# Optimization experiments

Measured on AMD Instinct MI355X. Metric: run time of the kernel, lower is better.

Reference implementation:

```python
import jax, jax.numpy as jnp
import numpy as np

B, D, K, C = 512, 256, 65536, 1000
T_SUP, T_DC, LS = 0.07, 0.1, 0.1
EPS = 1e-8


def _l2norm(x, axis):
    return x / jnp.linalg.norm(x, axis=axis, keepdims=True)


def setup_inputs() -> dict:
    key = jax.random.key(0)
    k1, k2, k3, k4, k5, k6, k7, k8 = jax.random.split(key, 8)
    norm_q = _l2norm(jax.random.normal(k1, (B, D), jnp.float32), axis=1)
    k_feat = _l2norm(jax.random.normal(k2, (B, D), jnp.float32), axis=1)
    q_logits = jax.random.normal(k3, (B, C), jnp.float32)
    logits_k = jax.random.normal(k4, (B, C), jnp.float32)
    queue = _l2norm(jax.random.normal(k5, (D, K), jnp.float32), axis=0)
    # queue_label_prob stores softmaxed class-probabilities column-wise (prob.T)
    queue_label_prob = jax.nn.softmax(jax.random.normal(k6, (C, K), jnp.float32), axis=0)
    queue_label = jax.random.randint(k7, (K,), 0, C, jnp.int64)
    target = jax.random.randint(k8, (B,), 0, C, jnp.int64)
    return {
        "norm_q": norm_q, "q_logits": q_logits, "k_feat": k_feat,
        "logits_k": logits_k, "queue": queue,
        "queue_label_prob": queue_label_prob, "queue_label": queue_label,
        "target": target, "knn_k": 200,
    }


def reference(norm_q, q_logits, k_feat, logits_k, queue, queue_label_prob,
              queue_label, target, knn_k):
    b = norm_q.shape[0]

    # ---- supcon_in ----
    sim = norm_q @ queue                                  # [B, K]
    _, idx = jax.lax.top_k(sim, knn_k)                    # [B, knn_k]
    sim_knn = jnp.take_along_axis(sim, idx, axis=1)
    w = jax.nn.softmax(sim_knn / T_SUP, axis=-1)
    pos = (target[:, None] == queue_label[idx])           # [B, knn_k]
    gt = jnp.sum(w * pos, axis=1)                         # [B]
    m = gt > EPS
    supin_loss = jnp.sum(jnp.where(m, -jnp.log(jnp.where(m, gt, 1.0)), 0.0)) / b

    # ---- label-smoothed onehot ----
    onehot = jnp.full((b, C), LS / (C - 1), jnp.float32)
    onehot = onehot.at[jnp.arange(b), target].set(1.0 - LS)

    log_q = jax.nn.log_softmax(q_logits, axis=1)
    q_mask = jax.nn.softmax(q_logits, axis=1).min(axis=1) > EPS  # [B]

    # ---- fc loss (masked CE with label smoothing) ----
    fc_loss = -jnp.sum(jnp.sum(onehot * log_q, axis=1) * q_mask) / b

    # ---- generate_dc_target (no-grad in original) ----
    sim_k = jax.nn.softmax((k_feat @ queue) / T_DC, axis=-1)      # [B, K]
    dc_target = sim_k @ queue_label_prob.T                        # [B, C]

    # ---- dc loss: KL(dc_target || softmax(q_logits)), masked, sum / B ----
    kl = jnp.where(dc_target > 0, dc_target * (jnp.log(jnp.where(dc_target > 0, dc_target, 1.0)) - log_q), 0.0)
    dc_loss = jnp.sum(jnp.sum(kl, axis=1) * q_mask) / b

    return (supin_loss, fc_loss, dc_loss)
```

## Files before the change

kernel.cpp:

```cpp
#include <hip/hip_runtime.h>
#include <math.h>

#define BN 512
#define DN 256
#define KN 65536
#define CN 1000
#define EQ_CAP 512
#define EPSTR 136

typedef __attribute__((ext_vector_type(8))) short bf16x8;
typedef __attribute__((ext_vector_type(4))) float f32x4;

__device__ __forceinline__ unsigned short f2bf(float f) {
    unsigned u = __float_as_uint(f);
    unsigned r = (u + 0x7FFFu + ((u >> 16) & 1u)) >> 16;
    return (unsigned short)r;
}
__device__ __forceinline__ float bf2f(unsigned short h) {
    return __uint_as_float(((unsigned)h) << 16);
}
__device__ __forceinline__ unsigned fkey16(unsigned b) {
    b &= 0xFFFFu;
    return (b & 0x8000u) ? ((~b) & 0xFFFFu) : (b | 0x8000u);
}
__device__ __forceinline__ void async16(const void* g, void* l) {
    __builtin_amdgcn_global_load_lds(
        (const __attribute__((address_space(1))) unsigned*)g,
        (__attribute__((address_space(3))) unsigned*)l, 16, 0, 0);
}
__device__ __forceinline__ unsigned cvtpk(float lo, float hi) {
    unsigned r;
    asm("v_cvt_pk_bf16_f32 %0, %1, %2" : "=v"(r) : "v"(lo), "v"(hi));
    return r;
}

__global__ void __launch_bounds__(256) cvt_bf16(const float* __restrict__ in,
                                                unsigned short* __restrict__ out) {
    int i = (blockIdx.x * 256 + threadIdx.x) * 4;
    float4 v = *(const float4*)&in[i];
    ushort4 o;
    o.x = f2bf(v.x); o.y = f2bf(v.y); o.z = f2bf(v.z); o.w = f2bf(v.w);
    *(ushort4*)&out[i] = o;
}

__global__ void __launch_bounds__(256) transpose_q(const float* __restrict__ Q,
                                                   unsigned short* __restrict__ Qt) {
    __shared__ float T[64][65];
    int tid = threadIdx.x;
    int n0 = blockIdx.x * 64;
    int d0 = blockIdx.y * 64;
    #pragma unroll
    for (int i = 0; i < 4; ++i) {
        int flat = i * 256 + tid;
        int d = flat >> 4, nq = (flat & 15) * 4;
        float4 v = *(const float4*)&Q[(size_t)(d0 + d) * KN + n0 + nq];
        T[d][nq] = v.x; T[d][nq + 1] = v.y; T[d][nq + 2] = v.z; T[d][nq + 3] = v.w;
    }
    __syncthreads();
    int n = tid >> 2, dbase = (tid & 3) * 16;
    unsigned u[8];
    #pragma unroll
    for (int j = 0; j < 8; ++j) {
        unsigned short a = f2bf(T[dbase + 2 * j][n]);
        unsigned short b = f2bf(T[dbase + 2 * j + 1][n]);
        u[j] = (unsigned)a | ((unsigned)b << 16);
    }
    unsigned short* o = &Qt[(size_t)(n0 + n) * DN + d0 + dbase];
    *(uint4*)o = make_uint4(u[0], u[1], u[2], u[3]);
    *(uint4*)(o + 8) = make_uint4(u[4], u[5], u[6], u[7]);
}

__global__ void __launch_bounds__(256) gemm_sim(const unsigned short* __restrict__ A,
                                                const unsigned short* __restrict__ Bt,
                                                unsigned short* __restrict__ simOut,
                                                unsigned short* __restrict__ expOut,
                                                float* __restrict__ Zb,
                                                int mBlockSplit) {
    __shared__ unsigned short smem[128 * 64 * 2];
    __shared__ float Zred[128];
    unsigned short* As = smem;
    unsigned short* Bs = smem + 128 * 64;
    int tid = threadIdx.x;
    int n0 = blockIdx.x * 128, m0 = blockIdx.y * 128;
    bool isExp = ((int)blockIdx.y >= mBlockSplit);
    int lane = tid & 63, w = tid >> 6;
    int l15 = lane & 15, quad = lane >> 4;
    int wm = w & 1, wn = w >> 1;
    f32x4 acc[4][4];
    #pragma unroll
    for (int mi = 0; mi < 4; ++mi)
        #pragma unroll
        for (int ni = 0; ni < 4; ++ni)
            #pragma unroll
            for (int j = 0; j < 4; ++j) acc[mi][ni][j] = 0.f;

    for (int k0 = 0; k0 < DN; k0 += 64) {
        #pragma unroll
        for (int i = 0; i < 4; ++i) {
            int f = (i * 256 + tid) * 8;
            async16(A + (size_t)(m0 + (f >> 6)) * DN + k0 + (f & 63), &As[f]);
        }
        #pragma unroll
        for (int i = 0; i < 4; ++i) {
            int f = (i * 256 + tid) * 8;
            async16(Bt + (size_t)(n0 + (f >> 6)) * DN + k0 + (f & 63), &Bs[f]);
        }
        __syncthreads();
        #pragma unroll
        for (int ks = 0; ks < 2; ++ks) {
            bf16x8 am[4], bn[4];
            #pragma unroll
            for (int mi = 0; mi < 4; ++mi)
                am[mi] = *(const bf16x8*)&As[(wm * 64 + mi * 16 + l15) * 64 + ks * 32 + quad * 8];
            #pragma unroll
            for (int ni = 0; ni < 4; ++ni)
                bn[ni] = *(const bf16x8*)&Bs[(wn * 64 + ni * 16 + l15) * 64 + ks * 32 + quad * 8];
            #pragma unroll
            for (int mi = 0; mi < 4; ++mi)
                #pragma unroll
                for (int ni = 0; ni < 4; ++ni)
                    acc[mi][ni] = __builtin_amdgcn_mfma_f32_16x16x32_bf16(bn[ni], am[mi], acc[mi][ni], 0, 0, 0);
        }
        __syncthreads();
    }

    unsigned short* obase = isExp ? expOut : simOut;
    int orow0 = isExp ? (m0 - mBlockSplit * 128) : m0;
    float rsum[4] = {0.f, 0.f, 0.f, 0.f};

    #pragma unroll
    for (int round = 0; round < 2; ++round) {
        if (wm == round) {
            #pragma unroll
            for (int mi = 0; mi < 4; ++mi) {
                int mrow = mi * 16 + l15;
                #pragma unroll
                for (int ni = 0; ni < 4; ++ni) {
                    int nc = wn * 64 + ni * 16 + quad * 4;
                    float v0 = acc[mi][ni][0], v1 = acc[mi][ni][1];
                    float v2 = acc[mi][ni][2], v3 = acc[mi][ni][3];
                    if (isExp) {
                        v0 = __expf(v0 * 10.0f); v1 = __expf(v1 * 10.0f);
                        v2 = __expf(v2 * 10.0f); v3 = __expf(v3 * 10.0f);
                    }
                    unsigned short u0 = f2bf(v0), u1 = f2bf(v1), u2 = f2bf(v2), u3 = f2bf(v3);
                    if (isExp) rsum[mi] += bf2f(u0) + bf2f(u1) + bf2f(u2) + bf2f(u3);
                    *(uint2*)&smem[mrow * EPSTR + nc] =
                        make_uint2((unsigned)u0 | ((unsigned)u1 << 16),
                                   (unsigned)u2 | ((unsigned)u3 << 16));
                }
            }
        }
        __syncthreads();
        #pragma unroll
        for (int j = 0; j < 4; ++j) {
            int fc = j * 256 + tid;
            int mr = fc >> 4;
            int ch = fc & 15;
            uint4 val = *(uint4*)&smem[mr * EPSTR + ch * 8];
            int g = orow0 + round * 64 + mr;
            *(uint4*)&obase[(size_t)g * KN + n0 + ch * 8] = val;
        }
        __syncthreads();
    }

    if (isExp) {
        float v4[4];
        #pragma unroll
        for (int mi = 0; mi < 4; ++mi) {
            float v = rsum[mi];
            v += __shfl_xor(v, 16, 64);
            v += __shfl_xor(v, 32, 64);
            v4[mi] = v;
        }
        if (wn == 0 && quad == 0) {
            #pragma unroll
            for (int mi = 0; mi < 4; ++mi) Zred[wm * 64 + mi * 16 + l15] = v4[mi];
        }
        __syncthreads();
        if (wn == 1 && quad == 0) {
            #pragma unroll
            for (int mi = 0; mi < 4; ++mi) Zred[wm * 64 + mi * 16 + l15] += v4[mi];
        }
        __syncthreads();
        if (tid < 128) atomicAdd(&Zb[orow0 + tid], Zred[tid]);
    }
}

__global__ void __launch_bounds__(256) supcon(const unsigned short* __restrict__ sim,
                                              const int* __restrict__ qlabel,
                                              const int* __restrict__ target,
                                              const int* __restrict__ knnp,
                                              float* __restrict__ out0) {
    __shared__ unsigned hist[4][256];
    __shared__ unsigned s_sel, s_cntAbove;
    __shared__ int eqIdx[EQ_CAP];
    __shared__ unsigned eqCount;
    __shared__ float redZ[256], redN[256];
    int tid = threadIdx.x, w = tid >> 6;
    int row = blockIdx.x;
    const unsigned short* srow = sim + (size_t)row * KN;
    int knn = *knnp;
    int tgt = target[row];
    if (tid == 0) { eqCount = 0u; }
    #pragma unroll
    for (int j = 0; j < 4; ++j) hist[j][tid] = 0u;
    __syncthreads();
    for (int i0 = tid * 4; i0 < KN; i0 += 1024) {
        uint2 v = *(const uint2*)&srow[i0];
        atomicAdd(&hist[w][fkey16(v.x) >> 8], 1u);
        atomicAdd(&hist[w][fkey16(v.x >> 16) >> 8], 1u);
        atomicAdd(&hist[w][fkey16(v.y) >> 8], 1u);
        atomicAdd(&hist[w][fkey16(v.y >> 16) >> 8], 1u);
    }
    __syncthreads();
    if (tid == 0) {
        unsigned acc = 0; int chosen = 0;
        for (int bin = 255; bin >= 0; --bin) {
            unsigned h = hist[0][bin] + hist[1][bin] + hist[2][bin] + hist[3][bin];
            if (acc + h >= (unsigned)knn) { chosen = bin; break; }
            acc += h;
        }
        s_cntAbove = acc; s_sel = (unsigned)chosen;
    }
    __syncthreads();
    unsigned selHi = s_sel;
    #pragma unroll
    for (int j = 0; j < 4; ++j) hist[j][tid] = 0u;
    __syncthreads();
    for (int i0 = tid * 4; i0 < KN; i0 += 1024) {
        uint2 v = *(const uint2*)&srow[i0];
        unsigned k0 = fkey16(v.x), k1 = fkey16(v.x >> 16), k2 = fkey16(v.y), k3 = fkey16(v.y >> 16);
        if ((k0 >> 8) == selHi) atomicAdd(&hist[w][k0 & 255u], 1u);
        if ((k1 >> 8) == selHi) atomicAdd(&hist[w][k1 & 255u], 1u);
        if ((k2 >> 8) == selHi) atomicAdd(&hist[w][k2 & 255u], 1u);
        if ((k3 >> 8) == selHi) atomicAdd(&hist[w][k3 & 255u], 1u);
    }
    __syncthreads();
    if (tid == 0) {
        unsigned acc = s_cntAbove; int chosen = 0;
        for (int bin = 255; bin >= 0; --bin) {
            unsigned h = hist[0][bin] + hist[1][bin] + hist[2][bin] + hist[3][bin];
            if (acc + h >= (unsigned)knn) { chosen = bin; break; }
            acc += h;
        }
        s_cntAbove = acc; s_sel = (selHi << 8) | (unsigned)chosen;
    }
    __syncthreads();
    unsigned tu = s_sel;
    unsigned cgt = s_cntAbove;
    const float invT = 1.0f / 0.07f;
    float Zl = 0.f, Nl = 0.f;
    for (int i0 = tid * 4; i0 < KN; i0 += 1024) {
        uint2 v = *(const uint2*)&srow[i0];
        unsigned bits[4] = {v.x & 0xFFFFu, v.x >> 16, v.y & 0xFFFFu, v.y >> 16};
        #pragma unroll
        for (int j = 0; j < 4; ++j) {
            unsigned u = fkey16(bits[j]);
            if (u > tu) {
                float e = __expf(bf2f((unsigned short)bits[j]) * invT);
                Zl += e;
                if (qlabel[i0 + j] == tgt) Nl += e;
            } else if (u == tu) {
                unsigned pos = atomicAdd(&eqCount, 1u);
                if (pos < EQ_CAP) eqIdx[pos] = i0 + j;
            }
        }
    }
    redZ[tid] = Zl; redN[tid] = Nl;
    __syncthreads();
    for (int s = 128; s > 0; s >>= 1) {
        if (tid < s) { redZ[tid] += redZ[tid + s]; redN[tid] += redN[tid + s]; }
        __syncthreads();
    }
    if (tid == 0) {
        float Z = redZ[0], num = redN[0];
        int neq = (int)(eqCount < (unsigned)EQ_CAP ? eqCount : (unsigned)EQ_CAP);
        int needed = knn - (int)cgt;
        if (needed > neq) needed = neq;
        for (int a = 1; a < neq; ++a) {
            int v = eqIdx[a]; int b2 = a - 1;
            while (b2 >= 0 && eqIdx[b2] > v) { eqIdx[b2 + 1] = eqIdx[b2]; --b2; }
            eqIdx[b2 + 1] = v;
        }
        unsigned tb = (tu & 0x8000u) ? (tu & 0x7FFFu) : ((~tu) & 0xFFFFu);
        float wt = __expf(bf2f((unsigned short)tb) * invT);
        for (int a = 0; a < needed; ++a) {
            Z += wt;
            if (qlabel[eqIdx[a]] == tgt) num += wt;
        }
        float gt = num / Z;
        if (gt > 1e-8f) atomicAdd(out0, -logf(gt) * (1.0f / (float)BN));
    }
}

__global__ void __launch_bounds__(256, 3) dc_gemm(const unsigned short* __restrict__ E,
                                                  const float* __restrict__ P,
                                                  float* __restrict__ dct) {
    __shared__ unsigned short As[128 * 64];
    __shared__ float Bsf[128 * 64];
    int tid = threadIdx.x;
    int c0 = blockIdx.x * 128, m0 = blockIdx.y * 128;
    int kb = blockIdx.z * (KN / 32);
    int lane = tid & 63, w = tid >> 6;
    int l15 = lane & 15, quad = lane >> 4;
    int wm = w & 1, wn = w >> 1;
    int tr = tid >> 3, chA = tid & 7;
    int sa = (chA ^ (tr & 7)) << 3;
    int br = tid >> 4, cbB = tid & 15;
    int sb = (cbB ^ (br & 7)) << 2;
    const int swr = l15 & 7;
    f32x4 acc[4][4];
    #pragma unroll
    for (int r = 0; r < 4; ++r)
        #pragma unroll
        for (int c = 0; c < 4; ++c)
            #pragma unroll
            for (int j = 0; j < 4; ++j) acc[r][c][j] = 0.f;

    for (int kc = 0; kc < KN / 32; kc += 64) {
        #pragma unroll
        for (int i = 0; i < 4; ++i) {
            int row = i * 32 + tr;
            async16(E + (size_t)(m0 + row) * KN + kb + kc + sa, &As[(i * 256 + tid) * 8]);
        }
        #pragma unroll
        for (int i = 0; i < 8; ++i) {
            int gr = c0 + i * 16 + br;
            if (gr > CN - 1) gr = CN - 1;
            async16(P + (size_t)gr * KN + kb + kc + sb, &Bsf[(i * 256 + tid) * 4]);
        }
        __syncthreads();
        #pragma unroll
        for (int ks = 0; ks < 2; ++ks) {
            bf16x8 af[4], bfr[4];
            #pragma unroll
            for (int r = 0; r < 4; ++r) {
                int arow = wm * 64 + r * 16 + l15;
                af[r] = *(const bf16x8*)&As[arow * 64 + (((ks * 4 + quad) ^ swr) << 3)];
            }
            #pragma unroll
            for (int c = 0; c < 4; ++c) {
                int brow = wn * 64 + c * 16 + l15;
                int ck = ks * 8 + quad * 2;
                float4 ra = *(const float4*)&Bsf[brow * 64 + ((ck ^ swr) << 2)];
                float4 rb = *(const float4*)&Bsf[brow * 64 + (((ck + 1) ^ swr) << 2)];
                uint4 pk;
                pk.x = cvtpk(ra.x, ra.y); pk.y = cvtpk(ra.z, ra.w);
                pk.z = cvtpk(rb.x, rb.y); pk.w = cvtpk(rb.z, rb.w);
                bfr[c] = *(bf16x8*)&pk;
            }
            #pragma unroll
            for (int r = 0; r < 4; ++r)
                #pragma unroll
                for (int c = 0; c < 4; ++c)
                    acc[r][c] = __builtin_amdgcn_mfma_f32_16x16x32_bf16(af[r], bfr[c], acc[r][c], 0, 0, 0);
        }
        __syncthreads();
    }
    #pragma unroll
    for (int r = 0; r < 4; ++r)
        #pragma unroll
        for (int reg = 0; reg < 4; ++reg) {
            int m = m0 + wm * 64 + r * 16 + quad * 4 + reg;
            #pragma unroll
            for (int c = 0; c < 4; ++c) {
                int cc = c0 + wn * 64 + c * 16 + l15;
                atomicAdd(&dct[m * 1024 + cc], acc[r][c][reg]);
            }
        }
}

__global__ void __launch_bounds__(256) logq_fc(const float* __restrict__ x_all,
                                               const int* __restrict__ target,
                                               float* __restrict__ logq,
                                               float* __restrict__ qmask,
                                               float* __restrict__ out1) {
    int row = blockIdx.x, tid = threadIdx.x;
    const float* x = x_all + (size_t)row * CN;
    __shared__ float red[256], red2[256];
    float mx = -INFINITY, mn = INFINITY;
    for (int c = tid; c < CN; c += 256) { float v = x[c]; mx = fmaxf(mx, v); mn = fminf(mn, v); }
    red[tid] = mx; red2[tid] = mn;
    __syncthreads();
    for (int s = 128; s > 0; s >>= 1) {
        if (tid < s) { red[tid] = fmaxf(red[tid], red[tid + s]); red2[tid] = fminf(red2[tid], red2[tid + s]); }
        __syncthreads();
    }
    mx = red[0]; mn = red2[0];
    __syncthreads();
    float se = 0.f, sx = 0.f;
    for (int c = tid; c < CN; c += 256) { float v = x[c]; se += __expf(v - mx); sx += v; }
    red[tid] = se; red2[tid] = sx;
    __syncthreads();
    for (int s = 128; s > 0; s >>= 1) {
        if (tid < s) { red[tid] += red[tid + s]; red2[tid] += red2[tid + s]; }
        __syncthreads();
    }
    float lse = mx + logf(red[0]);
    float sumlogq = red2[0] - (float)CN * lse;
    for (int c = tid; c < CN; c += 256) logq[(size_t)row * CN + c] = x[c] - lse;
    if (tid == 0) {
        float lqt = x[target[row]] - lse;
        bool qm = (mn - lse) > logf(1e-8f);
        qmask[row] = qm ? 1.0f : 0.0f;
        if (qm) {
            float fc = -(0.1f / 999.0f * (sumlogq - lqt) + 0.9f * lqt);
            atomicAdd(out1, fc * (1.0f / (float)BN));
        }
    }
}

__global__ void __launch_bounds__(256) dc_loss(const float* __restrict__ dct,
                                               const float* __restrict__ logq,
                                               const float* __restrict__ qmask,
                                               const float* __restrict__ Z,
                                               float* __restrict__ out2) {
    int row = blockIdx.x, tid = threadIdx.x;
    __shared__ float red[256];
    float invZ = 1.0f / Z[row];
    float s = 0.f;
    for (int c = tid; c < CN; c += 256) {
        float T = dct[row * 1024 + c] * invZ;
        if (T > 0.f) s += T * (logf(T) - logq[(size_t)row * CN + c]);
    }
    red[tid] = s;
    __syncthreads();
    for (int st = 128; st > 0; st >>= 1) {
        if (tid < st) red[tid] += red[tid + st];
        __syncthreads();
    }
    if (tid == 0 && qmask[row] > 0.f)
        atomicAdd(out2, red[0] * (1.0f / (float)BN));
}

extern "C" void kernel_launch(void* const* d_in, const int* in_sizes, int n_in,
                              void* d_out, int out_size, void* d_ws, size_t ws_size,
                              hipStream_t stream) {
    (void)in_sizes; (void)n_in; (void)out_size;
    const float* norm_q   = (const float*)d_in[0];
    const float* q_logits = (const float*)d_in[1];
    const float* k_feat   = (const float*)d_in[2];
    const float* queue    = (const float*)d_in[4];
    const float* qlp      = (const float*)d_in[5];
    const int*   qlabel   = (const int*)d_in[6];
    const int*   target   = (const int*)d_in[7];
    const int*   knnp     = (const int*)d_in[8];
    float* out = (float*)d_out;
    char* ws = (char*)d_ws;

    const size_t SIM_B = 67108864;
    const size_t QT_B  = 33554432;
    const size_t AC_B  = 524288;
    const size_t FUSED_NEED = SIM_B * 2 + QT_B + AC_B + 2097152 + 2048 + 2048000 + 2048;
    bool fused = (ws_size >= FUSED_NEED);

    unsigned short *simBF, *Ebf, *queueT, *Acat;
    float *dct, *Zb, *logq, *qmask;
    if (fused) {
        simBF  = (unsigned short*)(ws);
        Ebf    = (unsigned short*)(ws + SIM_B);
        queueT = (unsigned short*)(ws + 2 * SIM_B);
        Acat   = (unsigned short*)(ws + 2 * SIM_B + QT_B);
        dct    = (float*)(ws + 2 * SIM_B + QT_B + AC_B);
    } else {
        simBF  = (unsigned short*)(ws);
        Ebf    = simBF;
        queueT = (unsigned short*)(ws + SIM_B);
        Acat   = (unsigned short*)(ws + SIM_B + QT_B);
        dct    = (float*)(ws + SIM_B + QT_B + AC_B);
    }
    Zb    = (float*)((char*)dct + 2097152);
    logq  = (float*)((char*)Zb + 2048);
    qmask = (float*)((char*)logq + 2048000);

    hipMemsetAsync(dct, 0, 2097152 + 2048, stream);
    hipMemsetAsync(d_out, 0, 3 * sizeof(float), stream);

    cvt_bf16<<<dim3(128), 256, 0, stream>>>(norm_q, Acat);
    cvt_bf16<<<dim3(128), 256, 0, stream>>>(k_feat, Acat + (size_t)BN * DN);
    transpose_q<<<dim3(KN / 64, 4), 256, 0, stream>>>(queue, queueT);

    if (fused) {
        gemm_sim<<<dim3(KN / 128, 8), 256, 0, stream>>>(Acat, queueT, simBF, Ebf, Zb, 4);
        supcon<<<dim3(BN), 256, 0, stream>>>(simBF, qlabel, target, knnp, out + 0);
    } else {
        gemm_sim<<<dim3(KN / 128, 4), 256, 0, stream>>>(Acat, queueT, simBF, nullptr, nullptr, 4);
        supcon<<<dim3(BN), 256, 0, stream>>>(simBF, qlabel, target, knnp, out + 0);
        gemm_sim<<<dim3(KN / 128, 4), 256, 0, stream>>>(Acat + (size_t)BN * DN, queueT,
                                                        nullptr, Ebf, Zb, 0);
    }
    dc_gemm<<<dim3(8, 4, 32), 256, 0, stream>>>(Ebf, qlp, dct);
    logq_fc<<<dim3(BN), 256, 0, stream>>>(q_logits, target, logq, qmask, out + 1);
    dc_loss<<<dim3(BN), 256, 0, stream>>>(dct, logq, qmask, Zb, out + 2);
}
```

Measured before the change: 748.2 us.

## Double-buffer dc_gemm shared-memory tiles with a K-step of 32

Measured after the change: 851.0 us. 13.7% more time.

```diff
diff --git a/kernel.cpp b/kernel.cpp
--- a/kernel.cpp
+++ b/kernel.cpp
@@ -297,19 +297,18 @@
 __global__ void __launch_bounds__(256, 3) dc_gemm(const unsigned short* __restrict__ E,
                                                   const float* __restrict__ P,
                                                   float* __restrict__ dct) {
-    __shared__ unsigned short As[128 * 64];
-    __shared__ float Bsf[128 * 64];
+    __shared__ unsigned short As[2][128 * 32];
+    __shared__ float Bsf[2][128 * 32];
     int tid = threadIdx.x;
     int c0 = blockIdx.x * 128, m0 = blockIdx.y * 128;
     int kb = blockIdx.z * (KN / 32);
     int lane = tid & 63, w = tid >> 6;
     int l15 = lane & 15, quad = lane >> 4;
     int wm = w & 1, wn = w >> 1;
-    int tr = tid >> 3, chA = tid & 7;
-    int sa = (chA ^ (tr & 7)) << 3;
-    int br = tid >> 4, cbB = tid & 15;
-    int sb = (cbB ^ (br & 7)) << 2;
-    const int swr = l15 & 7;
+    int tr = tid >> 2, chA = tid & 3;
+    int sa = (chA ^ ((tr >> 1) & 3)) << 3;
+    int br = tid >> 3, cb = tid & 7;
+    int sb = (cb ^ (br & 7)) << 2;
     f32x4 acc[4][4];
     #pragma unroll
     for (int r = 0; r < 4; ++r)
@@ -318,44 +317,48 @@
             #pragma unroll
             for (int j = 0; j < 4; ++j) acc[r][c][j] = 0.f;
 
-    for (int kc = 0; kc < KN / 32; kc += 64) {
+    auto stage = [&](int buf, int kpos) {
+        #pragma unroll
+        for (int i = 0; i < 2; ++i)
+            async16(E + (size_t)(m0 + i * 64 + tr) * KN + kpos + sa,
+                    &As[buf][(i * 256 + tid) * 8]);
         #pragma unroll
         for (int i = 0; i < 4; ++i) {
-            int row = i * 32 + tr;
-            async16(E + (size_t)(m0 + row) * KN + kb + kc + sa, &As[(i * 256 + tid) * 8]);
-        }
-        #pragma unroll
-        for (int i = 0; i < 8; ++i) {
-            int gr = c0 + i * 16 + br;
+            int gr = c0 + i * 32 + br;
             if (gr > CN - 1) gr = CN - 1;
-            async16(P + (size_t)gr * KN + kb + kc + sb, &Bsf[(i * 256 + tid) * 4]);
-        }
-        __syncthreads();
-        #pragma unroll
-        for (int ks = 0; ks < 2; ++ks) {
-            bf16x8 af[4], bfr[4];
-            #pragma unroll
-            for (int r = 0; r < 4; ++r) {
-                int arow = wm * 64 + r * 16 + l15;
-                af[r] = *(const bf16x8*)&As[arow * 64 + (((ks * 4 + quad) ^ swr) << 3)];
-            }
-            #pragma unroll
-            for (int c = 0; c < 4; ++c) {
-                int brow = wn * 64 + c * 16 + l15;
-                int ck = ks * 8 + quad * 2;
-                float4 ra = *(const float4*)&Bsf[brow * 64 + ((ck ^ swr) << 2)];
-                float4 rb = *(const float4*)&Bsf[brow * 64 + (((ck + 1) ^ swr) << 2)];
-                uint4 pk;
-                pk.x = cvtpk(ra.x, ra.y); pk.y = cvtpk(ra.z, ra.w);
-                pk.z = cvtpk(rb.x, rb.y); pk.w = cvtpk(rb.z, rb.w);
-                bfr[c] = *(bf16x8*)&pk;
-            }
-            #pragma unroll
-            for (int r = 0; r < 4; ++r)
-                #pragma unroll
-                for (int c = 0; c < 4; ++c)
-                    acc[r][c] = __builtin_amdgcn_mfma_f32_16x16x32_bf16(af[r], bfr[c], acc[r][c], 0, 0, 0);
-        }
+            async16(P + (size_t)gr * KN + kpos + sb, &Bsf[buf][(i * 256 + tid) * 4]);
+        }
+    };
+
+    stage(0, kb);
+    __syncthreads();
+    for (int t = 0; t < 64; ++t) {
+        int cur = t & 1;
+        if (t < 63) stage(cur ^ 1, kb + (t + 1) * 32);
+        const unsigned short* Ab = As[cur];
+        const float* Bb = Bsf[cur];
+        bf16x8 af[4], bfr[4];
+        #pragma unroll
+        for (int r = 0; r < 4; ++r) {
+            int arow = wm * 64 + r * 16 + l15;
+            af[r] = *(const bf16x8*)&Ab[arow * 32 + ((quad ^ ((arow >> 1) & 3)) << 3)];
+        }
+        #pragma unroll
+        for (int c = 0; c < 4; ++c) {
+            int brow = wn * 64 + c * 16 + l15;
+            int k7 = brow & 7;
+            float4 ra = *(const float4*)&Bb[brow * 32 + (((quad * 2) ^ k7) << 2)];
+            float4 rb = *(const float4*)&Bb[brow * 32 + (((quad * 2 + 1) ^ k7) << 2)];
+            uint4 pk;
+            pk.x = cvtpk(ra.x, ra.y); pk.y = cvtpk(ra.z, ra.w);
+            pk.z = cvtpk(rb.x, rb.y); pk.w = cvtpk(rb.z, rb.w);
+            bfr[c] = *(bf16x8*)&pk;
+        }
+        #pragma unroll
+        for (int r = 0; r < 4; ++r)
+            #pragma unroll
+            for (int c = 0; c < 4; ++c)
+                acc[r][c] = __builtin_amdgcn_mfma_f32_16x16x32_bf16(af[r], bfr[c], acc[r][c], 0, 0, 0);
         __syncthreads();
     }
     #pragma unroll
```
